# Performance work log

Hardware: AMD Instinct MI355X
Metric: run time of the kernel (lower is better)

Reference implementation:

```python
import jax, jax.numpy as jnp
import numpy as np

K, D, P, C = 96, 256, 40, 8  # trials, embed dim, phoneme bins, gate hidden

def setup_inputs() -> dict:
    key = jax.random.key(0)
    ks = jax.random.split(key, 5)
    return {
        "enroll": jax.random.normal(ks[0], (K, D, P), jnp.float32),
        "test": jax.random.normal(ks[1], (K, D, P), jnp.float32),
        "fc1_w": jax.random.normal(ks[2], (C, 1), jnp.float32) * 0.5,
        "fc1_b": jax.random.normal(ks[3], (C,), jnp.float32) * 0.1,
        "fc2_w": jax.random.normal(ks[4], (1, C), jnp.float32) * 0.5,
    }

def _l2norm(x, axis):
    # torch F.normalize(p=2): x / max(||x||, eps)
    n = jnp.sqrt(jnp.sum(x * x, axis=axis, keepdims=True))
    return x / jnp.maximum(n, 1e-12)

def _gate(x, fc1_w, fc1_b, fc2_w):
    # tiny 1->C->1 MLP: fc2(tanh(fc1(x))), applied elementwise on x
    h = jnp.tanh(x[..., None] * fc1_w[:, 0] + fc1_b)   # [..., C]
    return jnp.einsum('...c,c->...', h, fc2_w[0])

def reference(enroll, test, fc1_w, fc1_b, fc2_w):
    e = _l2norm(enroll, axis=1)                        # [K, D, P]
    t = _l2norm(test, axis=1)                          # [K, D, P]
    # pho_matrix[k,l,i,j] = <e[k,:,i], t[l,:,j]>
    pho = jnp.einsum('kdi,ldj->klij', e, t)            # [K, K, P, P]
    cnt1 = jnp.sum(pho != 0, axis=-1).astype(pho.dtype) + 1e-6
    pho = _gate(pho, fc1_w, fc1_b, fc2_w) * pho        # gated elementwise
    pho = jnp.sum(pho, axis=-1) / cnt1                 # [K, K, P]
    cnt2 = jnp.sum(pho != 0, axis=-1).astype(pho.dtype) + 1e-6
    pho = _gate(pho, fc1_w, fc1_b, fc2_w) * pho        # [K, K, P]
    return jnp.sum(pho, axis=-1) / cnt2                # [K, K]
```

## Files before the change

### kernel.cpp

```cpp
#include <hip/hip_runtime.h>
#include <math.h>

#define KTR 96
#define DIM 256
#define PB  40
#define CH  8
#define MDIM 3840
#define KK  512
#define BM 160
#define BN 128
#define BK 32
#define LDA 40
#define NTAB 2113
#define TPAD 2120

typedef _Float16 v8h __attribute__((ext_vector_type(8)));
typedef float    v4f __attribute__((ext_vector_type(4)));

__device__ __forceinline__ float gate_ref(float x, const float* w, const float* b, const float* v) {
    float g = 0.f;
    #pragma unroll
    for (int c = 0; c < CH; ++c) g = fmaf(v[c], tanhf(fmaf(w[c], x, b[c])), g);
    return g;
}

__global__ __launch_bounds__(256) void k_norm(const float* __restrict__ enroll,
                                              const float* __restrict__ test,
                                              const float* __restrict__ fc1_w,
                                              const float* __restrict__ fc1_b,
                                              const float* __restrict__ fc2_w,
                                              _Float16* __restrict__ XT,
                                              _Float16* __restrict__ XE,
                                              float2* __restrict__ gtabG) {
    int b = blockIdx.x, tid = threadIdx.x;

    if (b >= 2 * KTR) {
        int i = (b - 2 * KTR) * 256 + tid;
        if (i < NTAB) {
            float w[CH], bb[CH], vv[CH];
            #pragma unroll
            for (int c = 0; c < CH; ++c) { w[c] = fc1_w[c]; bb[c] = fc1_b[c]; vv[c] = fc2_w[c]; }
            float g0 = gate_ref((float)(i - 1056) * 0.0009765625f, w, bb, vv);
            float g1 = gate_ref((float)(i - 1055) * 0.0009765625f, w, bb, vv);
            gtabG[i] = make_float2(g0, g1 - g0);
        }
        return;
    }

    bool isE = (b < KTR);
    int k = isE ? b : b - KTR;
    const float* src = (isE ? enroll : test) + (size_t)k * DIM * PB;

    __shared__ float S[DIM * 41];
    __shared__ float part[6 * PB];
    __shared__ float rn[PB];

    for (int i = tid; i < DIM * PB / 4; i += 256) {
        float4 v = ((const float4*)src)[i];
        int d = i / 10, c = i - d * 10;
        float* p = &S[d * 41 + c * 4];
        p[0] = v.x; p[1] = v.y; p[2] = v.z; p[3] = v.w;
    }
    __syncthreads();
    if (tid < 240) {
        int g = tid / PB, p = tid - (tid / PB) * PB;
        float acc = 0.f;
        for (int d = g; d < DIM; d += 6) {
            float x = S[d * 41 + p];
            acc = fmaf(x, x, acc);
        }
        part[g * PB + p] = acc;
    }
    __syncthreads();
    if (tid < PB) {
        float s = 0.f;
        #pragma unroll
        for (int g = 0; g < 6; ++g) s += part[g * PB + tid];
        rn[tid] = 1.0f / fmaxf(sqrtf(s), 1e-12f);
    }
    __syncthreads();

    int d = tid;
    for (int p = 0; p < PB; ++p) {
        float v = S[d * 41 + p] * rn[p];
        _Float16 h  = (_Float16)v;
        _Float16 lo = (_Float16)((v - (float)h) * 4096.0f);
        size_t m = (size_t)(k * PB + p);
        if (isE) { XE[m * KK + d] = lo; XE[m * KK + 256 + d] = h;  }
        else     { XT[m * KK + d] = h;  XT[m * KK + 256 + d] = lo; }
    }
}

__global__ __launch_bounds__(256, 3) void k_gemm(const _Float16* __restrict__ XT,
                                                 const _Float16* __restrict__ XE,
                                                 const float2* __restrict__ gtabG,
                                                 float* __restrict__ pho2) {
    __shared__ __align__(16) _Float16 LA[BM * LDA];
    __shared__ __align__(16) _Float16 LB[BN * LDA];
    __shared__ float gval[TPAD];
    __shared__ float gslope[TPAD];

    int tid  = threadIdx.x;
    int lane = tid & 63;
    int wv   = tid >> 6;

    for (int i = tid; i < NTAB; i += 256) {
        float2 t = gtabG[i];
        gval[i] = t.x; gslope[i] = t.y;
    }

    int m0 = blockIdx.y * BM;
    int n0 = blockIdx.x * BN;
    int wm = (wv & 1) * 80;
    int wn = (wv >> 1) * 64;
    int r15 = lane & 15;
    int q4  = lane >> 4;

    v4f acc[5][4];
    #pragma unroll
    for (int mt = 0; mt < 5; ++mt)
        #pragma unroll
        for (int nt = 0; nt < 4; ++nt)
            acc[mt][nt] = (v4f)0.f;

    int aoff[5], boff[4];
    #pragma unroll
    for (int mt = 0; mt < 5; ++mt) aoff[mt] = (wm + mt * 16 + r15) * LDA + q4 * 8;
    #pragma unroll
    for (int nt = 0; nt < 4; ++nt) boff[nt] = (wn + nt * 16 + r15) * LDA + q4 * 8;

    int arow = tid >> 2, aqc = tid & 3;
    const uint4* gT = (const uint4*)(XT + (size_t)(m0 + arow) * KK);
    const uint4* gE = (const uint4*)(XE + (size_t)(n0 + arow) * KK);
    uint4* lA = (uint4*)LA + (arow * 5 + aqc);
    uint4* lB = (uint4*)LB + (arow * 5 + aqc);

    uint4 va0, va1, va2, vb0, vb1;
    #define LOADS(IT) {                                                     \
        int ka = ((IT) < 16) ? (IT) * BK : ((IT) - 16) * BK;                \
        int kb = ((IT) < 16) ? (IT) * BK : 256 + ((IT) - 16) * BK;          \
        int ia = (ka >> 3) + aqc, ib = (kb >> 3) + aqc;                     \
        va0 = gT[ia]; va1 = gT[ia + 64 * 64];                               \
        if (tid < 128) va2 = gT[ia + 128 * 64];                             \
        vb0 = gE[ib]; vb1 = gE[ib + 64 * 64]; }

    LOADS(0);
    for (int it = 0; it < 24; ++it) {
        __syncthreads();
        lA[0]   = va0;
        lA[320] = va1;
        if (tid < 128) lA[640] = va2;
        lB[0]   = vb0;
        lB[320] = vb1;
        __syncthreads();

        if (it < 23) LOADS(it + 1);

        if (it == 16) {
            #pragma unroll
            for (int mt = 0; mt < 5; ++mt)
                #pragma unroll
                for (int nt = 0; nt < 4; ++nt)
                    acc[mt][nt] *= 0.000244140625f;
        }

        v8h af[5], bf[4];
        #pragma unroll
        for (int mt = 0; mt < 5; ++mt) af[mt] = *(const v8h*)(LA + aoff[mt]);
        #pragma unroll
        for (int nt = 0; nt < 4; ++nt) bf[nt] = *(const v8h*)(LB + boff[nt]);
        #pragma unroll
        for (int mt = 0; mt < 5; ++mt)
            #pragma unroll
            for (int nt = 0; nt < 4; ++nt)
                acc[mt][nt] = __builtin_amdgcn_mfma_f32_16x16x32_f16(af[mt], bf[nt], acc[mt][nt], 0, 0, 0);
    }
    #undef LOADS

    const float inv40 = 1.0f / (40.0f + 1e-6f);
    int lg = (m0 + wm) / PB;
    #pragma unroll
    for (int nt = 0; nt < 4; ++nt) {
        float s0 = 0.f, s1 = 0.f, t2 = 0.f;
        #pragma unroll
        for (int mt = 0; mt < 5; ++mt) {
            #pragma unroll
            for (int r = 0; r < 4; ++r) {
                float x = acc[mt][nt][r];
                float u = fmaf(x, 1024.0f, 1056.0f);
                int i = (int)u;
                i = min(max(i, 0), NTAB - 2);
                float f = u - (float)i;
                float g = fmaf(f, gslope[i], gval[i]);
                float xg = g * x;
                if (mt < 2)       s0 += xg;
                else if (mt == 2) t2 += xg;
                else              s1 += xg;
            }
        }
        bool lo = (q4 < 2);
        s0 += lo ? t2 : 0.f;
        s1 += lo ? 0.f : t2;
        s0 += __shfl_xor(s0, 16); s0 += __shfl_xor(s0, 32);
        s1 += __shfl_xor(s1, 16); s1 += __shfl_xor(s1, 32);
        if (q4 == 0) {
            int n = n0 + wn + nt * 16 + r15;
            int kk = n / PB, ii = n - kk * PB;
            pho2[((size_t)kk * KTR + lg)     * PB + ii] = s0 * inv40;
            pho2[((size_t)kk * KTR + lg + 1) * PB + ii] = s1 * inv40;
        }
    }
}

__global__ __launch_bounds__(256) void k_final(const float* __restrict__ pho2,
                                               const float* __restrict__ fc1_w,
                                               const float* __restrict__ fc1_b,
                                               const float* __restrict__ fc2_w,
                                               float* __restrict__ out) {
    int wv = threadIdx.x >> 6;
    int lane = threadIdx.x & 63;
    int pair = blockIdx.x * 4 + wv;

    float w[CH], bb[CH], vv[CH];
    #pragma unroll
    for (int c = 0; c < CH; ++c) { w[c] = fc1_w[c]; bb[c] = fc1_b[c]; vv[c] = fc2_w[c]; }

    float x = (lane < PB) ? pho2[(size_t)pair * PB + lane] : 0.f;
    float s = gate_ref(x, w, bb, vv) * x;

    #pragma unroll
    for (int off = 32; off; off >>= 1) s += __shfl_xor(s, off);
    if (lane == 0) out[pair] = s / (40.0f + 1e-6f);
}

extern "C" void kernel_launch(void* const* d_in, const int* in_sizes, int n_in,
                              void* d_out, int out_size, void* d_ws, size_t ws_size,
                              hipStream_t stream) {
    const float* enroll = (const float*)d_in[0];
    const float* test   = (const float*)d_in[1];
    const float* fc1_w  = (const float*)d_in[2];
    const float* fc1_b  = (const float*)d_in[3];
    const float* fc2_w  = (const float*)d_in[4];
    float* out = (float*)d_out;

    _Float16* XT = (_Float16*)d_ws;
    _Float16* XE = XT + (size_t)MDIM * KK;
    float* pho2  = (float*)(XE + (size_t)MDIM * KK);
    float2* gtabG = (float2*)(pho2 + (size_t)KTR * KTR * PB);

    k_norm<<<2 * KTR + 9, 256, 0, stream>>>(enroll, test, fc1_w, fc1_b, fc2_w, XT, XE, gtabG);
    dim3 g2(MDIM / BN, MDIM / BM);
    k_gemm<<<g2, 256, 0, stream>>>(XT, XE, gtabG, pho2);
    k_final<<<KTR * KTR / 4, 256, 0, stream>>>(pho2, fc1_w, fc1_b, fc2_w, out);
}
```

Measured before the change: 112.0 us.

## Fuse final gate into GEMM, double-buffer LDS via direct global-to-LDS loads

The second-stage gate and reduction move into the GEMM epilogue by retiling N to 120 columns (three whole enrollment trials per block), which removes the k_final launch and the pho2 round trip. The GEMM main loop now uses global_load_lds into a double-buffered LDS tile with one barrier per iteration instead of register staging. The normalisation kernel writes a pre-tiled 640-half row layout with vectorised 16-byte stores. The gate lookup table is read from global memory instead of being copied into LDS. In exchange, 8 of the 128 loaded B rows per block go unused and the table reads become scattered global loads.

```diff
diff --git a/kernel.cpp b/kernel.cpp
--- a/kernel.cpp
+++ b/kernel.cpp
@@ -6,16 +6,21 @@
 #define PB  40
 #define CH  8
 #define MDIM 3840
-#define KK  512
+#define ROWH 640
 #define BM 160
-#define BN 128
-#define BK 32
+#define BNS 128
+#define BNV 120
 #define LDA 40
+#define SZA (BM * LDA * 2)
+#define SZB (BNS * LDA * 2)
 #define NTAB 2113
-#define TPAD 2120
 
 typedef _Float16 v8h __attribute__((ext_vector_type(8)));
 typedef float    v4f __attribute__((ext_vector_type(4)));
+
+#define CP16(g, l) __builtin_amdgcn_global_load_lds(                  \
+    (const __attribute__((address_space(1))) void*)(g),               \
+    (__attribute__((address_space(3))) void*)(l), 16, 0, 0)
 
 __device__ __forceinline__ float gate_ref(float x, const float* w, const float* b, const float* v) {
     float g = 0.f;
@@ -40,8 +45,9 @@
             float w[CH], bb[CH], vv[CH];
             #pragma unroll
             for (int c = 0; c < CH; ++c) { w[c] = fc1_w[c]; bb[c] = fc1_b[c]; vv[c] = fc2_w[c]; }
-            float g0 = gate_ref((float)(i - 1056) * 0.0009765625f, w, bb, vv);
-            float g1 = gate_ref((float)(i - 1055) * 0.0009765625f, w, bb, vv);
+            float x0 = (float)(i - 1056) * 0.0009765625f;
+            float g0 = gate_ref(x0, w, bb, vv);
+            float g1 = gate_ref(x0 + 0.0009765625f, w, bb, vv);
             gtabG[i] = make_float2(g0, g1 - g0);
         }
         return;
@@ -80,41 +86,92 @@
     }
     __syncthreads();
 
-    int d = tid;
-    for (int p = 0; p < PB; ++p) {
-        float v = S[d * 41 + p] * rn[p];
-        _Float16 h  = (_Float16)v;
-        _Float16 lo = (_Float16)((v - (float)h) * 4096.0f);
-        size_t m = (size_t)(k * PB + p);
-        if (isE) { XE[m * KK + d] = lo; XE[m * KK + 256 + d] = h;  }
-        else     { XT[m * KK + d] = h;  XT[m * KK + 256 + d] = lo; }
-    }
+    _Float16* dst = isE ? XE : XT;
+    #pragma unroll
+    for (int i = 0; i < 5; ++i) {
+        int idx = tid + i * 256;
+        int p = idx >> 5, dg = idx & 31;
+        int d0 = dg * 8;
+        float r = rn[p];
+        union { _Float16 f[8]; uint4 u; } hv, lv;
+        #pragma unroll
+        for (int j = 0; j < 8; ++j) {
+            float x = S[(d0 + j) * 41 + p] * r;
+            _Float16 h = (_Float16)x;
+            hv.f[j] = h;
+            lv.f[j] = (_Float16)((x - (float)h) * 4096.0f);
+        }
+        int kc = dg >> 2, dd = (dg & 3) * 8;
+        size_t base = (size_t)(k * PB + p) * ROWH;
+        if (isE) {
+            *(uint4*)(dst + base + kc * 40 + dd)       = lv.u;
+            *(uint4*)(dst + base + (8 + kc) * 40 + dd) = hv.u;
+        } else {
+            *(uint4*)(dst + base + kc * 40 + dd)       = hv.u;
+            *(uint4*)(dst + base + (8 + kc) * 40 + dd) = lv.u;
+        }
+    }
+}
+
+struct Jobs {
+    const char* gA[4]; int lA[4]; bool aA[4];
+    const char* gB[3]; int lB[3]; bool aB[3];
+};
+
+__device__ __forceinline__ void issue(const Jobs& J, int it, int buf, void* LAp, void* LBp) {
+    int kA = (it < 16) ? it : it - 16;
+    int kB = (it < 16) ? it : it - 8;
+    char* la = (char*)LAp + buf * SZA;
+    char* lb = (char*)LBp + buf * SZB;
+    #pragma unroll
+    for (int j = 0; j < 4; ++j) if (J.aA[j]) CP16(J.gA[j] + kA * 80, la + J.lA[j]);
+    #pragma unroll
+    for (int j = 0; j < 3; ++j) if (J.aB[j]) CP16(J.gB[j] + kB * 80, lb + J.lB[j]);
 }
 
 __global__ __launch_bounds__(256, 3) void k_gemm(const _Float16* __restrict__ XT,
                                                  const _Float16* __restrict__ XE,
-                                                 const float2* __restrict__ gtabG,
-                                                 float* __restrict__ pho2) {
-    __shared__ __align__(16) _Float16 LA[BM * LDA];
-    __shared__ __align__(16) _Float16 LB[BN * LDA];
-    __shared__ float gval[TPAD];
-    __shared__ float gslope[TPAD];
-
-    int tid  = threadIdx.x;
-    int lane = tid & 63;
-    int wv   = tid >> 6;
-
-    for (int i = tid; i < NTAB; i += 256) {
-        float2 t = gtabG[i];
-        gval[i] = t.x; gslope[i] = t.y;
-    }
-
+                                                 const float2* __restrict__ gtab,
+                                                 const float* __restrict__ fc1_w,
+                                                 const float* __restrict__ fc1_b,
+                                                 const float* __restrict__ fc2_w,
+                                                 float* __restrict__ out) {
+    __shared__ __align__(16) _Float16 LA[2][BM * LDA];
+    __shared__ __align__(16) _Float16 LB[2][BNS * LDA];
+    __shared__ float ph2[4][132];
+
+    int tid = threadIdx.x, lane = tid & 63, wv = tid >> 6;
     int m0 = blockIdx.y * BM;
-    int n0 = blockIdx.x * BN;
+    int n0 = blockIdx.x * BNV;
+
+    Jobs J;
+    #pragma unroll
+    for (int j = 0; j < 4; ++j) {
+        int idx = tid + j * 256;
+        J.aA[j] = idx < BM * 5;
+        int row = idx / 5, c5 = idx - row * 5;
+        J.gA[j] = (const char*)XT + (size_t)(m0 + (J.aA[j] ? row : 0)) * (ROWH * 2) + c5 * 16;
+        J.lA[j] = idx * 16;
+    }
+    #pragma unroll
+    for (int j = 0; j < 3; ++j) {
+        int idx = tid + j * 256;
+        J.aB[j] = idx < BNS * 5;
+        int row = idx / 5, c5 = idx - row * 5;
+        int gr = n0 + row; if (gr > MDIM - 1) gr = MDIM - 1;
+        J.gB[j] = (const char*)XE + (size_t)(J.aB[j] ? gr : 0) * (ROWH * 2) + c5 * 16;
+        J.lB[j] = idx * 16;
+    }
+
     int wm = (wv & 1) * 80;
     int wn = (wv >> 1) * 64;
-    int r15 = lane & 15;
-    int q4  = lane >> 4;
+    int r15 = lane & 15, q4 = lane >> 4;
+
+    int aoff[5], boff[4];
+    #pragma unroll
+    for (int mt = 0; mt < 5; ++mt) aoff[mt] = (wm + mt * 16 + r15) * LDA + q4 * 8;
+    #pragma unroll
+    for (int nt = 0; nt < 4; ++nt) boff[nt] = (wn + nt * 16 + r15) * LDA + q4 * 8;
 
     v4f acc[5][4];
     #pragma unroll
@@ -123,38 +180,11 @@
         for (int nt = 0; nt < 4; ++nt)
             acc[mt][nt] = (v4f)0.f;
 
-    int aoff[5], boff[4];
-    #pragma unroll
-    for (int mt = 0; mt < 5; ++mt) aoff[mt] = (wm + mt * 16 + r15) * LDA + q4 * 8;
-    #pragma unroll
-    for (int nt = 0; nt < 4; ++nt) boff[nt] = (wn + nt * 16 + r15) * LDA + q4 * 8;
-
-    int arow = tid >> 2, aqc = tid & 3;
-    const uint4* gT = (const uint4*)(XT + (size_t)(m0 + arow) * KK);
-    const uint4* gE = (const uint4*)(XE + (size_t)(n0 + arow) * KK);
-    uint4* lA = (uint4*)LA + (arow * 5 + aqc);
-    uint4* lB = (uint4*)LB + (arow * 5 + aqc);
-
-    uint4 va0, va1, va2, vb0, vb1;
-    #define LOADS(IT) {                                                     \
-        int ka = ((IT) < 16) ? (IT) * BK : ((IT) - 16) * BK;                \
-        int kb = ((IT) < 16) ? (IT) * BK : 256 + ((IT) - 16) * BK;          \
-        int ia = (ka >> 3) + aqc, ib = (kb >> 3) + aqc;                     \
-        va0 = gT[ia]; va1 = gT[ia + 64 * 64];                               \
-        if (tid < 128) va2 = gT[ia + 128 * 64];                             \
-        vb0 = gE[ib]; vb1 = gE[ib + 64 * 64]; }
-
-    LOADS(0);
+    issue(J, 0, 0, LA, LB);
     for (int it = 0; it < 24; ++it) {
+        int buf = it & 1;
         __syncthreads();
-        lA[0]   = va0;
-        lA[320] = va1;
-        if (tid < 128) lA[640] = va2;
-        lB[0]   = vb0;
-        lB[320] = vb1;
-        __syncthreads();
-
-        if (it < 23) LOADS(it + 1);
+        if (it < 23) issue(J, it + 1, buf ^ 1, LA, LB);
 
         if (it == 16) {
             #pragma unroll
@@ -164,21 +194,22 @@
                     acc[mt][nt] *= 0.000244140625f;
         }
 
+        const _Float16* A = LA[buf];
+        const _Float16* B = LB[buf];
         v8h af[5], bf[4];
         #pragma unroll
-        for (int mt = 0; mt < 5; ++mt) af[mt] = *(const v8h*)(LA + aoff[mt]);
-        #pragma unroll
-        for (int nt = 0; nt < 4; ++nt) bf[nt] = *(const v8h*)(LB + boff[nt]);
+        for (int mt = 0; mt < 5; ++mt) af[mt] = *(const v8h*)(A + aoff[mt]);
+        #pragma unroll
+        for (int nt = 0; nt < 4; ++nt) bf[nt] = *(const v8h*)(B + boff[nt]);
         #pragma unroll
         for (int mt = 0; mt < 5; ++mt)
             #pragma unroll
             for (int nt = 0; nt < 4; ++nt)
                 acc[mt][nt] = __builtin_amdgcn_mfma_f32_16x16x32_f16(af[mt], bf[nt], acc[mt][nt], 0, 0, 0);
     }
-    #undef LOADS
 
     const float inv40 = 1.0f / (40.0f + 1e-6f);
-    int lg = (m0 + wm) / PB;
+    int lgb = wm / 40;
     #pragma unroll
     for (int nt = 0; nt < 4; ++nt) {
         float s0 = 0.f, s1 = 0.f, t2 = 0.f;
@@ -191,8 +222,8 @@
                 int i = (int)u;
                 i = min(max(i, 0), NTAB - 2);
                 float f = u - (float)i;
-                float g = fmaf(f, gslope[i], gval[i]);
-                float xg = g * x;
+                float2 tv = gtab[i];
+                float xg = fmaf(f, tv.y, tv.x) * x;
                 if (mt < 2)       s0 += xg;
                 else if (mt == 2) t2 += xg;
                 else              s1 += xg;
@@ -204,33 +235,26 @@
         s0 += __shfl_xor(s0, 16); s0 += __shfl_xor(s0, 32);
         s1 += __shfl_xor(s1, 16); s1 += __shfl_xor(s1, 32);
         if (q4 == 0) {
-            int n = n0 + wn + nt * 16 + r15;
-            int kk = n / PB, ii = n - kk * PB;
-            pho2[((size_t)kk * KTR + lg)     * PB + ii] = s0 * inv40;
-            pho2[((size_t)kk * KTR + lg + 1) * PB + ii] = s1 * inv40;
-        }
-    }
-}
-
-__global__ __launch_bounds__(256) void k_final(const float* __restrict__ pho2,
-                                               const float* __restrict__ fc1_w,
-                                               const float* __restrict__ fc1_b,
-                                               const float* __restrict__ fc2_w,
-                                               float* __restrict__ out) {
-    int wv = threadIdx.x >> 6;
-    int lane = threadIdx.x & 63;
-    int pair = blockIdx.x * 4 + wv;
-
-    float w[CH], bb[CH], vv[CH];
-    #pragma unroll
-    for (int c = 0; c < CH; ++c) { w[c] = fc1_w[c]; bb[c] = fc1_b[c]; vv[c] = fc2_w[c]; }
-
-    float x = (lane < PB) ? pho2[(size_t)pair * PB + lane] : 0.f;
-    float s = gate_ref(x, w, bb, vv) * x;
-
-    #pragma unroll
-    for (int off = 32; off; off >>= 1) s += __shfl_xor(s, off);
-    if (lane == 0) out[pair] = s / (40.0f + 1e-6f);
+            int col = wn + nt * 16 + r15;
+            ph2[lgb][col]     = s0 * inv40;
+            ph2[lgb + 1][col] = s1 * inv40;
+        }
+    }
+    __syncthreads();
+
+    float w2[CH], b2[CH], v2[CH];
+    #pragma unroll
+    for (int c = 0; c < CH; ++c) { w2[c] = fc1_w[c]; b2[c] = fc1_b[c]; v2[c] = fc2_w[c]; }
+
+    #pragma unroll
+    for (int r = 0; r < 3; ++r) {
+        float x = (lane < PB) ? ph2[wv][r * PB + lane] : 0.f;
+        float s = gate_ref(x, w2, b2, v2) * x;
+        #pragma unroll
+        for (int off = 32; off; off >>= 1) s += __shfl_xor(s, off);
+        if (lane == 0)
+            out[(size_t)(blockIdx.x * 3 + r) * KTR + blockIdx.y * 4 + wv] = s * inv40;
+    }
 }
 
 extern "C" void kernel_launch(void* const* d_in, const int* in_sizes, int n_in,
@@ -244,12 +268,10 @@
     float* out = (float*)d_out;
 
     _Float16* XT = (_Float16*)d_ws;
-    _Float16* XE = XT + (size_t)MDIM * KK;
-    float* pho2  = (float*)(XE + (size_t)MDIM * KK);
-    float2* gtabG = (float2*)(pho2 + (size_t)KTR * KTR * PB);
+    _Float16* XE = XT + (size_t)MDIM * ROWH;
+    float2* gtabG = (float2*)(XE + (size_t)MDIM * ROWH);
 
     k_norm<<<2 * KTR + 9, 256, 0, stream>>>(enroll, test, fc1_w, fc1_b, fc2_w, XT, XE, gtabG);
-    dim3 g2(MDIM / BN, MDIM / BM);
-    k_gemm<<<g2, 256, 0, stream>>>(XT, XE, gtabG, pho2);
-    k_final<<<KTR * KTR / 4, 256, 0, stream>>>(pho2, fc1_w, fc1_b, fc2_w, out);
-}
+    dim3 g2(MDIM / BNV, MDIM / BM);
+    k_gemm<<<g2, 256, 0, stream>>>(XT, XE, gtabG, fc1_w, fc1_b, fc2_w, out);
+}
```

Result: slower. 123.7 us (+10.5%).
